# Optimization experiments

Measured on AMD Instinct MI355X. Metric: run time of the kernel, lower is better.

## Reference

```python
import jax, jax.numpy as jnp
import numpy as np

D_MODEL = 256; N_HEADS = 8; N_LEVELS = 4; N_POINTS = 4; D_FFN = 1024
BS = 8; NQ = 100; NKPT = 17
LEVEL_SHAPES = [(160, 160), (80, 80), (40, 40), (20, 20)]  # (H, W) per level
LEN_V = sum(h * w for h, w in LEVEL_SHAPES)  # 34000


def layer_norm(x, g, b, eps=1e-5):
    m = x.mean(-1, keepdims=True)
    v = ((x - m) ** 2).mean(-1, keepdims=True)
    return (x - m) * jax.lax.rsqrt(v + eps) * g + b


def mha(q, k, v, Wqkv, bqkv, Wo, bo):
    # torch nn.MultiheadAttention, batch_first, eval mode (no dropout)
    d = q.shape[-1]; dh = d // N_HEADS
    def proj(x, W, b):
        return (x @ W.T + b).reshape(*x.shape[:-1], N_HEADS, dh)
    qp = proj(q, Wqkv[:d], bqkv[:d])
    kp = proj(k, Wqkv[d:2 * d], bqkv[d:2 * d])
    vp = proj(v, Wqkv[2 * d:], bqkv[2 * d:])
    att = jnp.einsum('bqhd,bkhd->bhqk', qp, kp) / jnp.sqrt(jnp.asarray(dh, q.dtype))
    att = jax.nn.softmax(att, -1)
    out = jnp.einsum('bhqk,bkhd->bqhd', att, vp).reshape(q.shape)
    return out @ Wo.T + bo


def bilinear_sample(val, loc, h, w):
    # val: (B, H, h*w, Dh); loc: (B, Lq, H, P, 2) normalized to [0,1]
    # matches F.grid_sample(align_corners=False, padding_mode='zeros') on grid 2*loc-1
    B, Lq, H, P, _ = loc.shape
    px = loc[..., 0] * w - 0.5
    py = loc[..., 1] * h - 0.5
    x0f = jnp.floor(px); y0f = jnp.floor(py)
    lx = px - x0f; ly = py - y0f
    x0 = x0f.astype(jnp.int32); y0 = y0f.astype(jnp.int32)
    out = jnp.zeros((B, H, Lq, P, val.shape[-1]), val.dtype)
    for dx, dy, wt in ((0, 0, (1 - lx) * (1 - ly)), (1, 0, lx * (1 - ly)),
                       (0, 1, (1 - lx) * ly), (1, 1, lx * ly)):
        xi = x0 + dx; yi = y0 + dy
        valid = ((xi >= 0) & (xi < w) & (yi >= 0) & (yi < h)).astype(val.dtype)
        idx = jnp.clip(yi, 0, h - 1) * w + jnp.clip(xi, 0, w - 1)  # (B,Lq,H,P)
        idx = idx.transpose(0, 2, 1, 3).reshape(B, H, Lq * P)
        g = jnp.take_along_axis(val, idx[..., None], axis=2).reshape(B, H, Lq, P, -1)
        out = out + g * (wt * valid).transpose(0, 2, 1, 3)[..., None]
    return out  # (B, H, Lq, P, Dh)


def ms_deform_attn(query, ref_points, memory, off_W, off_b, aw_W, aw_b,
                   val_W, val_b, outp_W, outp_b):
    B, Lq, _ = query.shape
    dh = D_MODEL // N_HEADS
    value = (memory @ val_W.T + val_b).reshape(B, LEN_V, N_HEADS, dh)
    off = (query @ off_W.T + off_b).reshape(B, Lq, N_HEADS, N_LEVELS, N_POINTS, 2)
    aw = (query @ aw_W.T + aw_b).reshape(B, Lq, N_HEADS, N_LEVELS * N_POINTS)
    aw = jax.nn.softmax(aw, -1).reshape(B, Lq, N_HEADS, N_LEVELS, N_POINTS)
    normalizer = jnp.array([[w, h] for h, w in LEVEL_SHAPES], dtype=query.dtype)  # (L,2) as (W,H)
    loc = ref_points[:, :, None, :, None, :] + off / normalizer[None, None, None, :, None, :]
    out = jnp.zeros((B, Lq, N_HEADS, dh), query.dtype)
    start = 0
    for l, (h, w) in enumerate(LEVEL_SHAPES):
        vl = value[:, start:start + h * w].transpose(0, 2, 1, 3)  # (B,H,hw,Dh)
        s = bilinear_sample(vl, loc[:, :, :, l], h, w)            # (B,H,Lq,P,Dh)
        out = out + jnp.einsum('bhqpd,bqhp->bqhd', s, aw[:, :, :, l])
        start += h * w
    return out.reshape(B, Lq, D_MODEL) @ outp_W.T + outp_b


def setup_inputs() -> dict:
    key = jax.random.key(0)
    ks = iter(jax.random.split(key, 40))
    d = D_MODEL
    def w(shape, s=0.02):
        return jax.random.normal(next(ks), shape, jnp.float32) * s
    inp = {
        'tgt_pose': jax.random.normal(next(ks), (BS, NQ, NKPT, d), jnp.float32),
        'tgt_pose_query_pos': jax.random.normal(next(ks), (BS, NQ, NKPT, d), jnp.float32),
        'tgt_pose_reference_points': jax.random.uniform(next(ks), (BS, NQ * NKPT, N_LEVELS, 2), jnp.float32),
        'memory': jax.random.normal(next(ks), (BS, LEN_V, d), jnp.float32),
        'win_Wqkv': w((3 * d, d)), 'win_bqkv': jnp.zeros((3 * d,), jnp.float32),
        'win_Wo': w((d, d)), 'win_bo': jnp.zeros((d,), jnp.float32),
        'win_ng': jnp.ones((d,), jnp.float32), 'win_nb': jnp.zeros((d,), jnp.float32),
        'acr_Wqkv': w((3 * d, d)), 'acr_bqkv': jnp.zeros((3 * d,), jnp.float32),
        'acr_Wo': w((d, d)), 'acr_bo': jnp.zeros((d,), jnp.float32),
        'acr_ng': jnp.ones((d,), jnp.float32), 'acr_nb': jnp.zeros((d,), jnp.float32),
        'off_W': w((N_HEADS * N_LEVELS * N_POINTS * 2, d)),
        'off_b': jax.random.uniform(next(ks), (N_HEADS * N_LEVELS * N_POINTS * 2,), jnp.float32, -1.0, 1.0),
        'aw_W': w((N_HEADS * N_LEVELS * N_POINTS, d)), 'aw_b': jnp.zeros((N_HEADS * N_LEVELS * N_POINTS,), jnp.float32),
        'val_W': w((d, d)), 'val_b': jnp.zeros((d,), jnp.float32),
        'outp_W': w((d, d)), 'outp_b': jnp.zeros((d,), jnp.float32),
        'gate_W': w((2 * d, 2 * d)), 'gate_b': jnp.zeros((2 * d,), jnp.float32),
        'gate_ng': jnp.ones((d,), jnp.float32), 'gate_nb': jnp.zeros((d,), jnp.float32),
        'ffn_W1': w((D_FFN, d)), 'ffn_b1': jnp.zeros((D_FFN,), jnp.float32),
        'ffn_W2': w((d, D_FFN)), 'ffn_b2': jnp.zeros((d,), jnp.float32),
        'n2_g': jnp.ones((d,), jnp.float32), 'n2_b': jnp.zeros((d,), jnp.float32),
        'memory_spatial_shapes': jnp.array(LEVEL_SHAPES, jnp.int32),
    }
    return inp


def reference(tgt_pose, tgt_pose_query_pos, tgt_pose_reference_points, memory,
              win_Wqkv, win_bqkv, win_Wo, win_bo, win_ng, win_nb,
              acr_Wqkv, acr_bqkv, acr_Wo, acr_bo, acr_ng, acr_nb,
              off_W, off_b, aw_W, aw_b, val_W, val_b, outp_W, outp_b,
              gate_W, gate_b, gate_ng, gate_nb,
              ffn_W1, ffn_b1, ffn_W2, ffn_b2, n2_g, n2_b,
              memory_spatial_shapes):
    bs, nq, K, d = tgt_pose.shape
    # with_pos_embed mutates tgt_pose in place in the torch code -> residual includes pos
    tgt = tgt_pose + tgt_pose_query_pos
    # within-attention over keypoints of each query
    x = tgt.reshape(bs * nq, K, d)
    t2 = mha(x, x, x, win_Wqkv, win_bqkv, win_Wo, win_bo).reshape(bs, nq, K, d)
    tgt = layer_norm(tgt + t2, win_ng, win_nb)
    # across-attention over queries for each keypoint
    xk = tgt.transpose(0, 2, 1, 3).reshape(bs * K, nq, d)
    t2 = mha(xk, xk, xk, acr_Wqkv, acr_bqkv, acr_Wo, acr_bo)
    tgt = layer_norm(xk + t2, acr_ng, acr_nb).reshape(bs, K, nq, d).transpose(0, 2, 1, 3)
    # second in-place pos add before deformable cross-attn (also feeds gateway)
    tgt_q = tgt + tgt_pose_query_pos
    t2 = ms_deform_attn(tgt_q.reshape(bs, nq * K, d), tgt_pose_reference_points, memory,
                        off_W, off_b, aw_W, aw_b, val_W, val_b, outp_W, outp_b)
    t2 = t2.reshape(bs, nq, K, d)
    # Gate
    g = jax.nn.sigmoid(jnp.concatenate([tgt_q, t2], -1) @ gate_W.T + gate_b)
    g1, g2 = jnp.split(g, 2, -1)
    tgt = layer_norm(g1 * tgt_q + g2 * t2, gate_ng, gate_nb)
    # FFN
    h = jax.nn.relu(tgt @ ffn_W1.T + ffn_b1)
    tgt = tgt + h @ ffn_W2.T + ffn_b2
    tgt = layer_norm(jnp.clip(tgt, -65504.0, 65504.0), n2_g, n2_b)
    return tgt
```

## Files before the change

### kernel.cpp

```cpp
#include <hip/hip_runtime.h>
#include <hip/hip_bf16.h>

#define NH 8
#define BS_ 8
#define NQ_ 100
#define NK_ 17
#define LQ 1700
#define T_TOK 13600
#define LEN_VV 34000

typedef __attribute__((ext_vector_type(8))) short short8v;
typedef __attribute__((ext_vector_type(8))) __bf16 bf16x8;
typedef __attribute__((ext_vector_type(4))) float f32x4;

__device__ __forceinline__ float wave_sum(float v){
#pragma unroll
  for (int m = 32; m; m >>= 1) v += __shfl_xor(v, m, 64);
  return v;
}
__device__ __forceinline__ short f2bf(float f){
  __hip_bfloat16 h = __float2bfloat16(f);
  return *reinterpret_cast<short*>(&h);
}
__device__ __forceinline__ float bf2f(short s){
  return __uint_as_float(((uint)(unsigned short)s) << 16);
}

template<int EPI, int ADDA, int SWZ>
__global__ __launch_bounds__(256) void mgemm_k(const float* __restrict__ A,
                                               const float* __restrict__ A2,
                                               const float* __restrict__ W,
                                               const float* __restrict__ bias,
                                               __hip_bfloat16* __restrict__ Cb,
                                               int M, int N, int K, int nbx){
  __shared__ short sh[128 * 136];
  short* As = sh;
  short* Ws = sh + 128 * 64;
  int j;
  if (SWZ){
    int total = gridDim.x;
    int q = total >> 3, r = total & 7;
    int x = blockIdx.x & 7, k = blockIdx.x >> 3;
    j = (x < r) ? x * (q + 1) + k : r * (q + 1) + (x - r) * q + k;
  } else {
    j = blockIdx.x;
  }
  const int tid = threadIdx.x;
  const int bm = (j / nbx) * 128, bn = (j % nbx) * 128;
  const int wave = tid >> 6, lane = tid & 63;
  const int wm = (wave >> 1) * 64, wn = (wave & 1) * 64;
  const int s = tid & 7;
  const int row0 = tid >> 3;
  f32x4 acc[4][4] = {};
  const int lrow = lane & 15, lk = lane >> 4;

  float4 ra[8], rw[8];
#pragma unroll
  for (int i = 0; i < 4; i++){
    int row = row0 + i * 32;
    int gr = bm + row;
    float4 z = make_float4(0.f, 0.f, 0.f, 0.f);
    if (gr < M){
      const float* p = A + (size_t)gr * K + s * 8;
      float4 x0 = ((const float4*)p)[0], x1 = ((const float4*)p)[1];
      if (ADDA){
        const float* q2 = A2 + (size_t)gr * K + s * 8;
        float4 y0 = ((const float4*)q2)[0], y1 = ((const float4*)q2)[1];
        x0.x+=y0.x; x0.y+=y0.y; x0.z+=y0.z; x0.w+=y0.w;
        x1.x+=y1.x; x1.y+=y1.y; x1.z+=y1.z; x1.w+=y1.w;
      }
      ra[2 * i] = x0; ra[2 * i + 1] = x1;
    } else { ra[2 * i] = z; ra[2 * i + 1] = z; }
    const float* q = W + (size_t)(bn + row) * K + s * 8;
    rw[2 * i] = ((const float4*)q)[0]; rw[2 * i + 1] = ((const float4*)q)[1];
  }

  for (int k0 = 0; k0 < K; k0 += 64){
#pragma unroll
    for (int i = 0; i < 4; i++){
      int row = row0 + i * 32;
      int sw = ((s ^ (row & 7)) << 3) + row * 64;
      float4 a0 = ra[2 * i], a1 = ra[2 * i + 1];
      short8v v;
      v[0]=f2bf(a0.x); v[1]=f2bf(a0.y); v[2]=f2bf(a0.z); v[3]=f2bf(a0.w);
      v[4]=f2bf(a1.x); v[5]=f2bf(a1.y); v[6]=f2bf(a1.z); v[7]=f2bf(a1.w);
      *(short8v*)&As[sw] = v;
      a0 = rw[2 * i]; a1 = rw[2 * i + 1];
      short8v u;
      u[0]=f2bf(a0.x); u[1]=f2bf(a0.y); u[2]=f2bf(a0.z); u[3]=f2bf(a0.w);
      u[4]=f2bf(a1.x); u[5]=f2bf(a1.y); u[6]=f2bf(a1.z); u[7]=f2bf(a1.w);
      *(short8v*)&Ws[sw] = u;
    }
    __syncthreads();
    if (k0 + 64 < K){
#pragma unroll
      for (int i = 0; i < 4; i++){
        int row = row0 + i * 32;
        int gr = bm + row;
        float4 z = make_float4(0.f, 0.f, 0.f, 0.f);
        if (gr < M){
          const float* p = A + (size_t)gr * K + k0 + 64 + s * 8;
          float4 x0 = ((const float4*)p)[0], x1 = ((const float4*)p)[1];
          if (ADDA){
            const float* q2 = A2 + (size_t)gr * K + k0 + 64 + s * 8;
            float4 y0 = ((const float4*)q2)[0], y1 = ((const float4*)q2)[1];
            x0.x+=y0.x; x0.y+=y0.y; x0.z+=y0.z; x0.w+=y0.w;
            x1.x+=y1.x; x1.y+=y1.y; x1.z+=y1.z; x1.w+=y1.w;
          }
          ra[2 * i] = x0; ra[2 * i + 1] = x1;
        } else { ra[2 * i] = z; ra[2 * i + 1] = z; }
        const float* q = W + (size_t)(bn + row) * K + k0 + 64 + s * 8;
        rw[2 * i] = ((const float4*)q)[0]; rw[2 * i + 1] = ((const float4*)q)[1];
      }
    }
#pragma unroll
    for (int ks = 0; ks < 2; ks++){
      short8v af[4], bw[4];
      int slot = ks * 4 + lk;
#pragma unroll
      for (int m = 0; m < 4; m++){
        int r = wm + m * 16 + lrow;
        af[m] = *(const short8v*)&As[r * 64 + ((slot ^ (r & 7)) << 3)];
      }
#pragma unroll
      for (int n = 0; n < 4; n++){
        int r = wn + n * 16 + lrow;
        bw[n] = *(const short8v*)&Ws[r * 64 + ((slot ^ (r & 7)) << 3)];
      }
#pragma unroll
      for (int m = 0; m < 4; m++)
#pragma unroll
        for (int n = 0; n < 4; n++)
          acc[m][n] = __builtin_amdgcn_mfma_f32_16x16x32_bf16(
              __builtin_bit_cast(bf16x8, af[m]),
              __builtin_bit_cast(bf16x8, bw[n]), acc[m][n], 0, 0, 0);
    }
    __syncthreads();
  }
  const int STR = 136;
#pragma unroll
  for (int n = 0; n < 4; n++){
    int col = wn + n * 16 + lrow;
    float bsv = bias[bn + col];
#pragma unroll
    for (int m = 0; m < 4; m++){
#pragma unroll
      for (int i = 0; i < 4; i++){
        int row = wm + m * 16 + lk * 4 + i;
        float c = acc[m][n][i] + bsv;
        if (EPI == 1) c = fmaxf(c, 0.f);
        sh[row * STR + col] = f2bf(c);
      }
    }
  }
  __syncthreads();
#pragma unroll
  for (int it = 0; it < 8; it++){
    int r = it * 16 + (tid >> 4);
    int chunk = tid & 15;
    if (bm + r < M){
      uint4 v = *(const uint4*)((const char*)sh + r * 272 + chunk * 16);
      *(uint4*)((char*)Cb + ((size_t)(bm + r) * N + bn) * 2 + chunk * 16) = v;
    }
  }
}

template<int EPI, int OUTB, int INB, int DUALA>
__global__ __launch_bounds__(256) void g64_k(const void* __restrict__ Av,
                                             const void* __restrict__ A1v,
                                             const float* __restrict__ W0,
                                             const float* __restrict__ W1,
                                             int NSPLIT,
                                             const float* __restrict__ bias0,
                                             const float* __restrict__ bias1,
                                             const float* __restrict__ RES,
                                             float* __restrict__ Cf,
                                             __hip_bfloat16* __restrict__ Cb,
                                             int M, int N, int K, int sA){
  __shared__ short sh64[2 * 64 * 64];
  short* As = sh64;
  short* Ws = sh64 + 64 * 64;
  const int tid = threadIdx.x;
  const int bn = blockIdx.x * 64, bm = blockIdx.y * 64;
  const int wave = tid >> 6, lane = tid & 63;
  const int wm = (wave >> 1) * 32, wn = (wave & 1) * 32;
  const int s = tid & 7, row0 = tid >> 3;
  const int lrow = lane & 15, lk = lane >> 4;
  f32x4 acc[2][2] = {};

  for (int k0 = 0; k0 < K; k0 += 64){
#pragma unroll
    for (int i = 0; i < 2; i++){
      int row = row0 + i * 32;
      int sw = ((s ^ (row & 7)) << 3) + row * 64;
      short8v v = {};
      int gr = bm + row;
      if (gr < M){
        if (INB){
          v = *(const short8v*)((const short*)Av + (size_t)gr * sA + k0 + s * 8);
        } else {
          const float* Ap;
          if (DUALA) Ap = (k0 < 256) ? (const float*)Av + (size_t)gr * 256 + k0
                                     : (const float*)A1v + (size_t)gr * 256 + (k0 - 256);
          else Ap = (const float*)Av + (size_t)gr * sA + k0;
          float4 a0 = ((const float4*)(Ap + s * 8))[0];
          float4 a1 = ((const float4*)(Ap + s * 8))[1];
          v[0]=f2bf(a0.x); v[1]=f2bf(a0.y); v[2]=f2bf(a0.z); v[3]=f2bf(a0.w);
          v[4]=f2bf(a1.x); v[5]=f2bf(a1.y); v[6]=f2bf(a1.z); v[7]=f2bf(a1.w);
        }
      }
      *(short8v*)&As[sw] = v;
      int wr = bn + row;
      const float* Wp = (wr < NSPLIT) ? W0 + (size_t)wr * K + k0
                                      : W1 + (size_t)(wr - NSPLIT) * K + k0;
      float4 b0 = ((const float4*)(Wp + s * 8))[0];
      float4 b1 = ((const float4*)(Wp + s * 8))[1];
      short8v u;
      u[0]=f2bf(b0.x); u[1]=f2bf(b0.y); u[2]=f2bf(b0.z); u[3]=f2bf(b0.w);
      u[4]=f2bf(b1.x); u[5]=f2bf(b1.y); u[6]=f2bf(b1.z); u[7]=f2bf(b1.w);
      *(short8v*)&Ws[sw] = u;
    }
    __syncthreads();
#pragma unroll
    for (int ks = 0; ks < 2; ks++){
      int slot = ks * 4 + lk;
      short8v af[2], bw[2];
#pragma unroll
      for (int m = 0; m < 2; m++){
        int r = wm + m * 16 + lrow;
        af[m] = *(const short8v*)&As[r * 64 + ((slot ^ (r & 7)) << 3)];
      }
#pragma unroll
      for (int n = 0; n < 2; n++){
        int r = wn + n * 16 + lrow;
        bw[n] = *(const short8v*)&Ws[r * 64 + ((slot ^ (r & 7)) << 3)];
      }
#pragma unroll
      for (int m = 0; m < 2; m++)
#pragma unroll
        for (int n = 0; n < 2; n++)
          acc[m][n] = __builtin_amdgcn_mfma_f32_16x16x32_bf16(
              __builtin_bit_cast(bf16x8, af[m]),
              __builtin_bit_cast(bf16x8, bw[n]), acc[m][n], 0, 0, 0);
    }
    __syncthreads();
  }
  if (OUTB){
    const int STR = 72;
#pragma unroll
    for (int n = 0; n < 2; n++){
      int col = wn + n * 16 + lrow;
      int gc = bn + col;
      float bsv = (gc < NSPLIT) ? bias0[gc] : bias1[gc - NSPLIT];
#pragma unroll
      for (int m = 0; m < 2; m++){
#pragma unroll
        for (int i = 0; i < 4; i++){
          int row = wm + m * 16 + lk * 4 + i;
          float c = acc[m][n][i] + bsv;
          if (EPI == 1) c = fmaxf(c, 0.f);
          if (EPI == 2) c = 1.f / (1.f + expf(-c));
          sh64[row * STR + col] = f2bf(c);
        }
      }
    }
    __syncthreads();
#pragma unroll
    for (int it = 0; it < 2; it++){
      int r = it * 32 + (tid >> 3);
      int chunk = tid & 7;
      if (bm + r < M){
        uint4 v = *(const uint4*)((const char*)sh64 + r * 144 + chunk * 16);
        *(uint4*)((char*)Cb + ((size_t)(bm + r) * N + bn) * 2 + chunk * 16) = v;
      }
    }
  } else {
#pragma unroll
    for (int n = 0; n < 2; n++){
      int gc = bn + wn + n * 16 + lrow;
      float bsv = (gc < NSPLIT) ? bias0[gc] : bias1[gc - NSPLIT];
#pragma unroll
      for (int m = 0; m < 2; m++){
#pragma unroll
        for (int i = 0; i < 4; i++){
          int row = bm + wm + m * 16 + lk * 4 + i;
          if (row >= M) continue;
          float c = acc[m][n][i] + bsv;
          if (EPI == 1) c = fmaxf(c, 0.f);
          if (EPI == 2) c = 1.f / (1.f + expf(-c));
          if (EPI == 3) c += RES[(size_t)row * N + gc];
          Cf[(size_t)row * N + gc] = c;
        }
      }
    }
  }
}

template<int TP, int NSPL>
__global__ __launch_bounds__(256) void mha_mfma_k(const short* __restrict__ qkv,
                                                  __hip_bfloat16* __restrict__ out, int S){
  constexpr int MT = TP / 16;
  constexpr int KSTEPS = (TP + 31) / 32;
  constexpr int KS32 = KSTEPS * 32;
  constexpr int VSTRB = (KS32 == 128) ? 256 : 128;
  constexpr int CH = (MT + NSPL - 1) / NSPL;
  __shared__ short QK[2][TP][64];
  __shared__ short Vt[2][32][VSTRB / 2];
  __shared__ float Sc[2][16][128];
  __shared__ float rinv[2][16];

  const int tid = threadIdx.x;
  const int bid = blockIdx.x;
  const int batch = bid / (4 * NSPL);
  const int rem = bid % (4 * NSPL);
  const int hp = rem / NSPL;
  const int half = rem % NSPL;
  const int mtlo = half * CH;
  const int mthi = (mtlo + CH < MT) ? (mtlo + CH) : MT;
  const int wave = tid >> 6, lane = tid & 63;
  const int hh = wave >> 1, wsub = wave & 1;
  const int lrow = lane & 15, lk = lane >> 4;
  const float scale = 0.17677669529663687f;
  const size_t qbase = (size_t)batch * S * 768;

  for (int idx = tid; idx < 2 * TP * 4; idx += 256){
    int h2 = idx >= TP * 4;
    int rm = idx - h2 * TP * 4;
    int j = rm >> 2, s = rm & 3;
    int h = hp * 2 + h2;
    short8v qv = {}, kv = {};
    if (j < S){
      const short* p = qkv + qbase + (size_t)j * 768 + h * 32 + s * 8;
      qv = *(const short8v*)p;
      kv = *(const short8v*)(p + 256);
    }
    *(short8v*)&QK[h2][j][(s ^ (j & 7)) << 3] = qv;
    *(short8v*)&QK[h2][j][((s + 4) ^ (j & 7)) << 3] = kv;
  }
  for (int idx = tid; idx < 2 * KS32 * 4; idx += 256){
    int h2 = idx >= KS32 * 4;
    int rm = idx - h2 * KS32 * 4;
    int j = rm >> 2, e8 = rm & 3;
    int h = hp * 2 + h2;
    short8v v = {};
    if (j < S) v = *(const short8v*)(qkv + qbase + (size_t)j * 768 + h * 32 + 512 + e8 * 8);
#pragma unroll
    for (int c = 0; c < 8; c++){
      int e = e8 * 8 + c;
      char* pb = (char*)&Vt[h2][0][0] + e * VSTRB + (((j >> 3) ^ (e & 7)) << 4) + ((j & 7) << 1);
      *(short*)pb = v[c];
    }
  }
  __syncthreads();

  for (int mt = mtlo; mt < mthi; mt++){
    for (int nt = wsub; nt < MT; nt += 2){
      int ar = mt * 16 + lrow;
      short8v aq = *(const short8v*)&QK[hh][ar][(lk ^ (ar & 7)) << 3];
      int br = nt * 16 + lrow;
      short8v bk = *(const short8v*)&QK[hh][br][((lk + 4) ^ (br & 7)) << 3];
      f32x4 z = {};
      f32x4 d = __builtin_amdgcn_mfma_f32_16x16x32_bf16(
          __builtin_bit_cast(bf16x8, aq), __builtin_bit_cast(bf16x8, bk), z, 0, 0, 0);
#pragma unroll
      for (int i = 0; i < 4; i++){
        int rr = lk * 4 + i;
        int c = nt * 16 + lrow;
        Sc[hh][rr][(((c >> 2) ^ (rr & 7)) << 2) + (c & 3)] = d[i] * scale;
      }
    }
    __syncthreads();
    if (wsub == 0){
      int rr = lane >> 2, p = lane & 3;
      int grow = mt * 16 + rr;
      int Seff = (grow < S) ? S : 0;
      float mx = -1e30f;
#pragma unroll
      for (int m = 0; m < KSTEPS; m++){
        int j = p + 4 * m;
#pragma unroll
        for (int hf = 0; hf < 2; hf++){
          int ls = 2 * j + hf;
          float4 v = *(const float4*)&Sc[hh][rr][(ls ^ (rr & 7)) << 2];
          int c0 = ls * 4;
          mx = fmaxf(mx, (c0 + 0 < Seff) ? v.x : -1e30f);
          mx = fmaxf(mx, (c0 + 1 < Seff) ? v.y : -1e30f);
          mx = fmaxf(mx, (c0 + 2 < Seff) ? v.z : -1e30f);
          mx = fmaxf(mx, (c0 + 3 < Seff) ? v.w : -1e30f);
        }
      }
      mx = fmaxf(mx, __shfl_xor(mx, 1, 64));
      mx = fmaxf(mx, __shfl_xor(mx, 2, 64));
      float sum = 0.f;
#pragma unroll
      for (int m = 0; m < KSTEPS; m++){
        int j = p + 4 * m;
        float ev[8];
#pragma unroll
        for (int hf = 0; hf < 2; hf++){
          int ls = 2 * j + hf;
          float4 v = *(const float4*)&Sc[hh][rr][(ls ^ (rr & 7)) << 2];
          int c0 = ls * 4;
          ev[hf * 4 + 0] = (c0 + 0 < Seff) ? __expf(v.x - mx) : 0.f;
          ev[hf * 4 + 1] = (c0 + 1 < Seff) ? __expf(v.y - mx) : 0.f;
          ev[hf * 4 + 2] = (c0 + 2 < Seff) ? __expf(v.z - mx) : 0.f;
          ev[hf * 4 + 3] = (c0 + 3 < Seff) ? __expf(v.w - mx) : 0.f;
        }
        short8v pb;
#pragma unroll
        for (int q2 = 0; q2 < 8; q2++){ pb[q2] = f2bf(ev[q2]); sum += ev[q2]; }
        *(short8v*)((char*)&Sc[hh][rr][0] + ((j ^ (rr & 7)) << 4)) = pb;
      }
      sum += __shfl_xor(sum, 1, 64);
      sum += __shfl_xor(sum, 2, 64);
      if (p == 0) rinv[hh][rr] = (sum > 0.f) ? 1.f / sum : 0.f;
    }
    __syncthreads();
    {
      int nt2 = wsub;
      f32x4 acc = {};
#pragma unroll
      for (int ks = 0; ks < KSTEPS; ks++){
        int slot = ks * 4 + lk;
        short8v ap = *(const short8v*)((const char*)&Sc[hh][lrow][0] + ((slot ^ (lrow & 7)) << 4));
        int e = nt2 * 16 + lrow;
        short8v bv = *(const short8v*)((const char*)&Vt[hh][0][0] + e * VSTRB + ((slot ^ (e & 7)) << 4));
        acc = __builtin_amdgcn_mfma_f32_16x16x32_bf16(
            __builtin_bit_cast(bf16x8, ap), __builtin_bit_cast(bf16x8, bv), acc, 0, 0, 0);
      }
      int h = hp * 2 + hh;
#pragma unroll
      for (int i = 0; i < 4; i++){
        int row = mt * 16 + lk * 4 + i;
        if (row < S){
          float rv = rinv[hh][lk * 4 + i];
          out[((size_t)batch * S + row) * 256 + h * 32 + nt2 * 16 + lrow] =
              __float2bfloat16(acc[i] * rv);
        }
      }
    }
    __syncthreads();
  }
}

template<int MODE>
__global__ __launch_bounds__(64) void ln_k(const float* __restrict__ a,
                                           const float* __restrict__ b,
                                           const float* __restrict__ g,
                                           const float* __restrict__ be,
                                           float* __restrict__ out,
                                           const float* __restrict__ qpre,
                                           const float* __restrict__ qpost){
  int r = blockIdx.x;
  int lane = threadIdx.x;
  float4 xa = *(const float4*)(a + (size_t)r * 256 + lane * 4);
  float x[4] = { xa.x, xa.y, xa.z, xa.w };
  if (MODE != 5){
    float4 xb = *(const float4*)(b + (size_t)r * 256 + lane * 4);
    x[0] += xb.x; x[1] += xb.y; x[2] += xb.z; x[3] += xb.w;
  }
  if (MODE == 4){
    float4 xq = *(const float4*)(qpre + (size_t)r * 256 + lane * 4);
    x[0] += xq.x; x[1] += xq.y; x[2] += xq.z; x[3] += xq.w;
  }
  if (MODE == 5){
#pragma unroll
    for (int i = 0; i < 4; i++) x[i] = fminf(fmaxf(x[i], -65504.f), 65504.f);
  }
  float s = x[0] + x[1] + x[2] + x[3];
  s = wave_sum(s);
  float mean = s * (1.f / 256.f);
  float sq = 0.f;
#pragma unroll
  for (int i = 0; i < 4; i++){ float d = x[i] - mean; sq += d * d; }
  float var = wave_sum(sq) * (1.f / 256.f);
  float rstd = rsqrtf(var + 1e-5f);
  float4 gg = *(const float4*)(g + lane * 4);
  float4 bb = *(const float4*)(be + lane * 4);
  size_t orow = r;
  if (MODE == 3){
    int bi = r / LQ; int rem = r % LQ; int kk = rem / NQ_; int q = rem % NQ_;
    orow = (size_t)bi * LQ + q * NK_ + kk;
  }
  if (MODE == 4){
    int bi = r / LQ; int rem = r % LQ; int q = rem / NK_; int kk = rem % NK_;
    orow = (size_t)bi * LQ + kk * NQ_ + q;
  }
  float4 o;
  o.x = (x[0] - mean) * rstd * gg.x + bb.x;
  o.y = (x[1] - mean) * rstd * gg.y + bb.y;
  o.z = (x[2] - mean) * rstd * gg.z + bb.z;
  o.w = (x[3] - mean) * rstd * gg.w + bb.w;
  if (MODE == 3){
    float4 qv = *(const float4*)(qpost + orow * 256 + lane * 4);
    o.x += qv.x; o.y += qv.y; o.z += qv.z; o.w += qv.w;
  }
  *(float4*)(out + orow * 256 + lane * 4) = o;
}

__global__ __launch_bounds__(64) void gate_ln_k(const short* __restrict__ G,
                                                const float* __restrict__ aq,
                                                const float* __restrict__ t2,
                                                const float* __restrict__ g,
                                                const float* __restrict__ be,
                                                float* __restrict__ out){
  int r = blockIdx.x;
  int lane = threadIdx.x;
  const short* gp = G + (size_t)r * 512 + lane * 4;
  float g1v[4], g2v[4];
#pragma unroll
  for (int i = 0; i < 4; i++){ g1v[i] = bf2f(gp[i]); g2v[i] = bf2f(gp[256 + i]); }
  float4 xa = *(const float4*)(aq + (size_t)r * 256 + lane * 4);
  float4 xt = *(const float4*)(t2 + (size_t)r * 256 + lane * 4);
  float x[4] = { g1v[0] * xa.x + g2v[0] * xt.x, g1v[1] * xa.y + g2v[1] * xt.y,
                 g1v[2] * xa.z + g2v[2] * xt.z, g1v[3] * xa.w + g2v[3] * xt.w };
  float s = x[0] + x[1] + x[2] + x[3];
  s = wave_sum(s);
  float mean = s * (1.f / 256.f);
  float sq = 0.f;
#pragma unroll
  for (int i = 0; i < 4; i++){ float d = x[i] - mean; sq += d * d; }
  float var = wave_sum(sq) * (1.f / 256.f);
  float rstd = rsqrtf(var + 1e-5f);
  float4 gg = *(const float4*)(g + lane * 4);
  float4 bb = *(const float4*)(be + lane * 4);
  float4 o;
  o.x = (x[0] - mean) * rstd * gg.x + bb.x;
  o.y = (x[1] - mean) * rstd * gg.y + bb.y;
  o.z = (x[2] - mean) * rstd * gg.z + bb.z;
  o.w = (x[3] - mean) * rstd * gg.w + bb.w;
  *(float4*)(out + (size_t)r * 256 + lane * 4) = o;
}

__global__ __launch_bounds__(256) void deform_k(const __hip_bfloat16* __restrict__ val,
                                                const float* __restrict__ offaw,
                                                const float* __restrict__ ref,
                                                unsigned int* __restrict__ outb){
  __shared__ uint2 meta[32][16][4];
  const int tid = threadIdx.x;
  const int t0 = blockIdx.x * 4;
  {
    int g = tid >> 3;
    int pair = tid & 7;
    int lt = g >> 3, h = g & 7;
    int t = t0 + lt;
    int b = t / LQ;
    int p0 = pair * 2;
    int l = p0 >> 2;
    const int starts[4] = {0, 25600, 32000, 33600};
    const int HS[4] = {160, 80, 40, 20};
    int w = HS[l];
    const float* ap = offaw + (size_t)t * 384 + 256 + h * 16;
    float a0 = ap[p0];
    float a1 = ap[p0 + 1];
    float mx = fmaxf(a0, a1);
#pragma unroll
    for (int m = 1; m <= 4; m <<= 1) mx = fmaxf(mx, __shfl_xor(mx, m, 64));
    float e0 = expf(a0 - mx), e1 = expf(a1 - mx);
    float s = e0 + e1;
#pragma unroll
    for (int m = 1; m <= 4; m <<= 1) s += __shfl_xor(s, m, 64);
    float inv = 1.f / s;
    float rx = ref[((size_t)t * 4 + l) * 2 + 0];
    float ry = ref[((size_t)t * 4 + l) * 2 + 1];
    float4 ov = *(const float4*)(offaw + (size_t)t * 384 + h * 32 + l * 8 + p0 * 2);
    int vbase = (b * LEN_VV + starts[l]) * 128 + h * 16;
#pragma unroll
    for (int pp = 0; pp < 2; pp++){
      float wgt = (pp ? e1 : e0) * inv;
      float px = rx * w + (pp ? ov.z : ov.x) - 0.5f;
      float py = ry * w + (pp ? ov.w : ov.y) - 0.5f;
      float x0f = floorf(px), y0f = floorf(py);
      float lx = px - x0f, ly = py - y0f;
      int x0 = (int)x0f, y0 = (int)y0f;
#pragma unroll
    for (int c = 0; c < 4; c++){
        int dx = c & 1, dy = c >> 1;
        int xi = x0 + dx, yi = y0 + dy;
        bool ok = (xi >= 0) & (xi < w) & (yi >= 0) & (yi < w);
        float cw = ok ? wgt * (dx ? lx : 1.f - lx) * (dy ? ly : 1.f - ly) : 0.f;
        uint idx = ok ? (uint)(vbase + (yi * w + xi) * 128) : 0u;
        uint2 m2; m2.x = idx; m2.y = __float_as_uint(cw);
        meta[g][p0 + pp][c] = m2;
      }
    }
  }
  __syncthreads();
  const uint* V2 = (const uint*)val;
  int sg = tid >> 4, lane = tid & 15;
#pragma unroll
  for (int it = 0; it < 2; it++){
    int g = it * 16 + sg;
    int lt = g >> 3, h = g & 7;
    int t = t0 + lt;
    float ax = 0.f, ay = 0.f;
#pragma unroll 4
    for (int c = 0; c < 64; c++){
      uint2 mw = meta[g][c >> 2][c & 3];
      float wv = __uint_as_float(mw.y);
      uint v = V2[(size_t)mw.x + lane];
      float lo = __uint_as_float(v << 16);
      float hi = __uint_as_float(v & 0xffff0000u);
      ax += wv * lo;
      ay += wv * hi;
    }
    uint u = ((uint)(unsigned short)f2bf(ay) << 16) | (uint)(unsigned short)f2bf(ax);
    outb[((size_t)t * 256 + h * 32) / 2 + lane] = u;
  }
}

extern "C" void kernel_launch(void* const* d_in, const int* in_sizes, int n_in,
                              void* d_out, int out_size, void* d_ws, size_t ws_size,
                              hipStream_t stream){
  const float* tgt_pose = (const float*)d_in[0];
  const float* qpos     = (const float*)d_in[1];
  const float* refp     = (const float*)d_in[2];
  const float* memory   = (const float*)d_in[3];
  const float* win_Wqkv = (const float*)d_in[4];
  const float* win_bqkv = (const float*)d_in[5];
  const float* win_Wo   = (const float*)d_in[6];
  const float* win_bo   = (const float*)d_in[7];
  const float* win_ng   = (const float*)d_in[8];
  const float* win_nb   = (const float*)d_in[9];
  const float* acr_Wqkv = (const float*)d_in[10];
  const float* acr_bqkv = (const float*)d_in[11];
  const float* acr_Wo   = (const float*)d_in[12];
  const float* acr_bo   = (const float*)d_in[13];
  const float* acr_ng   = (const float*)d_in[14];
  const float* acr_nb   = (const float*)d_in[15];
  const float* off_W    = (const float*)d_in[16];
  const float* off_b    = (const float*)d_in[17];
  const float* aw_W     = (const float*)d_in[18];
  const float* aw_b     = (const float*)d_in[19];
  const float* val_W    = (const float*)d_in[20];
  const float* val_b    = (const float*)d_in[21];
  const float* outp_W   = (const float*)d_in[22];
  const float* outp_b   = (const float*)d_in[23];
  const float* gate_W   = (const float*)d_in[24];
  const float* gate_b   = (const float*)d_in[25];
  const float* gate_ng  = (const float*)d_in[26];
  const float* gate_nb  = (const float*)d_in[27];
  const float* ffn_W1   = (const float*)d_in[28];
  const float* ffn_b1   = (const float*)d_in[29];
  const float* ffn_W2   = (const float*)d_in[30];
  const float* ffn_b2   = (const float*)d_in[31];
  const float* n2_g     = (const float*)d_in[32];
  const float* n2_b     = (const float*)d_in[33];

  float* out = (float*)d_out;
  char* ws = (char*)d_ws;
  const size_t TB = (size_t)T_TOK * 256 * 4;
  float* B0 = (float*)(ws);
  float* B1 = (float*)(ws + TB);
  float* B2 = (float*)(ws + 2 * TB);
  float* B3 = (float*)(ws + 3 * TB);
  char* p = ws + 4 * TB;
  short* Qb = (short*)p;                 p += (size_t)T_TOK * 768 * 2;
  short* ABF = (short*)p;                p += (size_t)T_TOK * 256 * 2;
  float* OFFAW = (float*)p;              p += (size_t)T_TOK * 384 * 4;
  short* Gb = (short*)p;                 p += (size_t)T_TOK * 512 * 2;
  char* Vregion = p;
  __hip_bfloat16* V = (__hip_bfloat16*)Vregion;
  short* FF = (short*)Vregion;

  const int GM128 = (T_TOK + 127) / 128;
  const int GM64  = (T_TOK + 63) / 64;
  const int BIG = 1 << 30;

  mgemm_k<0,0,1><<<2 * 2125, 256, 0, stream>>>(memory, nullptr, val_W, val_b, V, BS_ * LEN_VV, 256, 256, 2);
  mgemm_k<0,1,0><<<6 * GM128, 256, 0, stream>>>(tgt_pose, qpos, win_Wqkv, win_bqkv, (__hip_bfloat16*)Qb, T_TOK, 768, 256, 6);
  mha_mfma_k<32,1><<<800 * 4, 256, 0, stream>>>(Qb, (__hip_bfloat16*)ABF, 17);
  g64_k<0,0,1,0><<<dim3(4, GM64), 256, 0, stream>>>(ABF, nullptr, win_Wo, win_Wo, BIG, win_bo, win_bo, nullptr, B2, nullptr, T_TOK, 256, 256, 256);
  ln_k<4><<<T_TOK, 64, 0, stream>>>(tgt_pose, B2, win_ng, win_nb, B1, qpos, nullptr);
  mgemm_k<0,0,0><<<6 * GM128, 256, 0, stream>>>(B1, nullptr, acr_Wqkv, acr_bqkv, (__hip_bfloat16*)Qb, T_TOK, 768, 256, 6);
  mha_mfma_k<112,2><<<136 * 8, 256, 0, stream>>>(Qb, (__hip_bfloat16*)ABF, 100);
  g64_k<0,0,1,0><<<dim3(4, GM64), 256, 0, stream>>>(ABF, nullptr, acr_Wo, acr_Wo, BIG, acr_bo, acr_bo, nullptr, B2, nullptr, T_TOK, 256, 256, 256);
  ln_k<3><<<T_TOK, 64, 0, stream>>>(B1, B2, acr_ng, acr_nb, B0, nullptr, qpos);
  g64_k<0,0,0,0><<<dim3(6, GM64), 256, 0, stream>>>(B0, nullptr, off_W, aw_W, 256, off_b, aw_b, nullptr, OFFAW, nullptr, T_TOK, 384, 256, 256);
  deform_k<<<T_TOK / 4, 256, 0, stream>>>(V, OFFAW, refp, (unsigned int*)ABF);
  g64_k<0,0,1,0><<<dim3(4, GM64), 256, 0, stream>>>(ABF, nullptr, outp_W, outp_W, BIG, outp_b, outp_b, nullptr, B3, nullptr, T_TOK, 256, 256, 256);
  g64_k<2,1,0,1><<<dim3(8, GM64), 256, 0, stream>>>(B0, B3, gate_W, gate_W, BIG, gate_b, gate_b, nullptr, nullptr, (__hip_bfloat16*)Gb, T_TOK, 512, 512, 256);
  gate_ln_k<<<T_TOK, 64, 0, stream>>>(Gb, B0, B3, gate_ng, gate_nb, B2);
  mgemm_k<1,0,0><<<8 * GM128, 256, 0, stream>>>(B2, nullptr, ffn_W1, ffn_b1, (__hip_bfloat16*)FF, T_TOK, 1024, 256, 8);
  g64_k<3,0,1,0><<<dim3(4, GM64), 256, 0, stream>>>(FF, nullptr, ffn_W2, ffn_W2, BIG, ffn_b2, ffn_b2, B2, B1, nullptr, T_TOK, 256, 1024, 1024);
  ln_k<5><<<T_TOK, 64, 0, stream>>>(B1, nullptr, n2_g, n2_b, out, nullptr, nullptr);
}
```

Before: 472.6 us.

## Fuse output-projection GEMMs with residual LayerNorm and widen deform gather loads

Adds a 512-thread GEMM kernel whose block computes a full 256-wide output row tile, then applies bias, residual adds, optional clamp, LayerNorm and the transposed row remap in the epilogue. It replaces three GEMM plus LayerNorm kernel pairs, removing the fp32 intermediate round-trip and three launches. It also changes the deform sampling gather so each lane loads 4 bf16 values (uint2) with 8 lanes per head instead of 2 values with 16 lanes. Risks: the fused kernel launches only one block per 64 rows (about 213 blocks), so there is less parallelism, it converts fp32 weights to bf16 inside every block, and it computes variance with the single-pass E[x²]−mean² formula.

```diff
diff --git a/kernel.cpp b/kernel.cpp
--- a/kernel.cpp
+++ b/kernel.cpp
@@ -296,6 +296,148 @@
   }
 }
 
+template<int SITE>
+__global__ __launch_bounds__(512) void gln_k(const short* __restrict__ Abf,
+                                             const float* __restrict__ W,
+                                             const float* __restrict__ bias,
+                                             const float* __restrict__ r0,
+                                             const float* __restrict__ r1,
+                                             const float* __restrict__ g,
+                                             const float* __restrict__ be,
+                                             float* __restrict__ out,
+                                             int M, int K){
+  __shared__ short As[64 * 64];
+  __shared__ short Ws[256 * 64];
+  __shared__ float part[64][4][2];
+  __shared__ float stats[64][2];
+  const int tid = threadIdx.x;
+  const int bm = blockIdx.x * 64;
+  const int wave = tid >> 6, lane = tid & 63;
+  const int wm = (wave >> 2) * 32, wn = (wave & 3) * 64;
+  const int s = tid & 7, row0 = tid >> 3;
+  const int lrow = lane & 15, lk = lane >> 4;
+  f32x4 acc[2][4] = {};
+
+  short8v pa = {};
+  { int gr = bm + row0; if (gr < M) pa = *(const short8v*)(Abf + (size_t)gr * K + s * 8); }
+  float4 pw[8];
+#pragma unroll
+  for (int i = 0; i < 4; i++){
+    const float* wp = W + (size_t)(row0 + i * 64) * K + s * 8;
+    pw[2 * i] = ((const float4*)wp)[0]; pw[2 * i + 1] = ((const float4*)wp)[1];
+  }
+
+  for (int k0 = 0; k0 < K; k0 += 64){
+    *(short8v*)&As[row0 * 64 + ((s ^ (row0 & 7)) << 3)] = pa;
+#pragma unroll
+    for (int i = 0; i < 4; i++){
+      int row = row0 + i * 64;
+      float4 b0 = pw[2 * i], b1 = pw[2 * i + 1];
+      short8v u;
+      u[0]=f2bf(b0.x); u[1]=f2bf(b0.y); u[2]=f2bf(b0.z); u[3]=f2bf(b0.w);
+      u[4]=f2bf(b1.x); u[5]=f2bf(b1.y); u[6]=f2bf(b1.z); u[7]=f2bf(b1.w);
+      *(short8v*)&Ws[row * 64 + ((s ^ (row & 7)) << 3)] = u;
+    }
+    __syncthreads();
+    if (k0 + 64 < K){
+      int gr = bm + row0;
+      pa = (short8v){};
+      if (gr < M) pa = *(const short8v*)(Abf + (size_t)gr * K + k0 + 64 + s * 8);
+#pragma unroll
+      for (int i = 0; i < 4; i++){
+        const float* wp = W + (size_t)(row0 + i * 64) * K + k0 + 64 + s * 8;
+        pw[2 * i] = ((const float4*)wp)[0]; pw[2 * i + 1] = ((const float4*)wp)[1];
+      }
+    }
+#pragma unroll
+    for (int ks = 0; ks < 2; ks++){
+      int slot = ks * 4 + lk;
+      short8v af[2], bw[4];
+#pragma unroll
+      for (int m = 0; m < 2; m++){
+        int r = wm + m * 16 + lrow;
+        af[m] = *(const short8v*)&As[r * 64 + ((slot ^ (r & 7)) << 3)];
+      }
+#pragma unroll
+      for (int n = 0; n < 4; n++){
+        int r = wn + n * 16 + lrow;
+        bw[n] = *(const short8v*)&Ws[r * 64 + ((slot ^ (r & 7)) << 3)];
+      }
+#pragma unroll
+      for (int m = 0; m < 2; m++)
+#pragma unroll
+        for (int n = 0; n < 4; n++)
+          acc[m][n] = __builtin_amdgcn_mfma_f32_16x16x32_bf16(
+              __builtin_bit_cast(bf16x8, af[m]),
+              __builtin_bit_cast(bf16x8, bw[n]), acc[m][n], 0, 0, 0);
+    }
+    __syncthreads();
+  }
+
+#pragma unroll
+  for (int m = 0; m < 2; m++){
+#pragma unroll
+    for (int i = 0; i < 4; i++){
+      int row = wm + m * 16 + lk * 4 + i;
+      int grow = bm + row;
+      float s1 = 0.f, s2 = 0.f;
+      if (grow < M){
+#pragma unroll
+        for (int n = 0; n < 4; n++){
+          int col = wn + n * 16 + lrow;
+          float x = acc[m][n][i] + bias[col] + r0[(size_t)grow * 256 + col];
+          if (SITE == 0) x += r1[(size_t)grow * 256 + col];
+          if (SITE == 2) x = fminf(fmaxf(x, -65504.f), 65504.f);
+          acc[m][n][i] = x;
+          s1 += x; s2 += x * x;
+        }
+      }
+#pragma unroll
+      for (int msk = 1; msk <= 8; msk <<= 1){
+        s1 += __shfl_xor(s1, msk, 64);
+        s2 += __shfl_xor(s2, msk, 64);
+      }
+      if (lrow == 0){ part[row][wave & 3][0] = s1; part[row][wave & 3][1] = s2; }
+    }
+  }
+  __syncthreads();
+  if (tid < 64){
+    float s1 = part[tid][0][0] + part[tid][1][0] + part[tid][2][0] + part[tid][3][0];
+    float s2 = part[tid][0][1] + part[tid][1][1] + part[tid][2][1] + part[tid][3][1];
+    float mean = s1 * (1.f / 256.f);
+    float var = s2 * (1.f / 256.f) - mean * mean;
+    stats[tid][0] = mean;
+    stats[tid][1] = rsqrtf(fmaxf(var, 0.f) + 1e-5f);
+  }
+  __syncthreads();
+#pragma unroll
+  for (int m = 0; m < 2; m++){
+#pragma unroll
+    for (int i = 0; i < 4; i++){
+      int row = wm + m * 16 + lk * 4 + i;
+      int grow = bm + row;
+      if (grow >= M) continue;
+      float mean = stats[row][0], rstd = stats[row][1];
+      size_t orow = grow;
+      if (SITE == 0){
+        int bi = grow / LQ; int rem = grow % LQ; int q = rem / NK_; int kk = rem % NK_;
+        orow = (size_t)bi * LQ + kk * NQ_ + q;
+      }
+      if (SITE == 1){
+        int bi = grow / LQ; int rem = grow % LQ; int kk = rem / NQ_; int q = rem % NQ_;
+        orow = (size_t)bi * LQ + q * NK_ + kk;
+      }
+#pragma unroll
+      for (int n = 0; n < 4; n++){
+        int col = wn + n * 16 + lrow;
+        float o = (acc[m][n][i] - mean) * rstd * g[col] + be[col];
+        if (SITE == 1) o += r1[orow * 256 + col];
+        out[orow * 256 + col] = o;
+      }
+    }
+  }
+}
+
 template<int TP, int NSPL>
 __global__ __launch_bounds__(256) void mha_mfma_k(const short* __restrict__ qkv,
                                                   __hip_bfloat16* __restrict__ out, int S){
@@ -441,61 +583,6 @@
     }
     __syncthreads();
   }
-}
-
-template<int MODE>
-__global__ __launch_bounds__(64) void ln_k(const float* __restrict__ a,
-                                           const float* __restrict__ b,
-                                           const float* __restrict__ g,
-                                           const float* __restrict__ be,
-                                           float* __restrict__ out,
-                                           const float* __restrict__ qpre,
-                                           const float* __restrict__ qpost){
-  int r = blockIdx.x;
-  int lane = threadIdx.x;
-  float4 xa = *(const float4*)(a + (size_t)r * 256 + lane * 4);
-  float x[4] = { xa.x, xa.y, xa.z, xa.w };
-  if (MODE != 5){
-    float4 xb = *(const float4*)(b + (size_t)r * 256 + lane * 4);
-    x[0] += xb.x; x[1] += xb.y; x[2] += xb.z; x[3] += xb.w;
-  }
-  if (MODE == 4){
-    float4 xq = *(const float4*)(qpre + (size_t)r * 256 + lane * 4);
-    x[0] += xq.x; x[1] += xq.y; x[2] += xq.z; x[3] += xq.w;
-  }
-  if (MODE == 5){
-#pragma unroll
-    for (int i = 0; i < 4; i++) x[i] = fminf(fmaxf(x[i], -65504.f), 65504.f);
-  }
-  float s = x[0] + x[1] + x[2] + x[3];
-  s = wave_sum(s);
-  float mean = s * (1.f / 256.f);
-  float sq = 0.f;
-#pragma unroll
-  for (int i = 0; i < 4; i++){ float d = x[i] - mean; sq += d * d; }
-  float var = wave_sum(sq) * (1.f / 256.f);
-  float rstd = rsqrtf(var + 1e-5f);
-  float4 gg = *(const float4*)(g + lane * 4);
-  float4 bb = *(const float4*)(be + lane * 4);
-  size_t orow = r;
-  if (MODE == 3){
-    int bi = r / LQ; int rem = r % LQ; int kk = rem / NQ_; int q = rem % NQ_;
-    orow = (size_t)bi * LQ + q * NK_ + kk;
-  }
-  if (MODE == 4){
-    int bi = r / LQ; int rem = r % LQ; int q = rem / NK_; int kk = rem % NK_;
-    orow = (size_t)bi * LQ + kk * NQ_ + q;
-  }
-  float4 o;
-  o.x = (x[0] - mean) * rstd * gg.x + bb.x;
-  o.y = (x[1] - mean) * rstd * gg.y + bb.y;
-  o.z = (x[2] - mean) * rstd * gg.z + bb.z;
-  o.w = (x[3] - mean) * rstd * gg.w + bb.w;
-  if (MODE == 3){
-    float4 qv = *(const float4*)(qpost + orow * 256 + lane * 4);
-    o.x += qv.x; o.y += qv.y; o.z += qv.z; o.w += qv.w;
-  }
-  *(float4*)(out + orow * 256 + lane * 4) = o;
 }
 
 __global__ __launch_bounds__(64) void gate_ln_k(const short* __restrict__ G,
@@ -574,7 +661,7 @@
       float lx = px - x0f, ly = py - y0f;
       int x0 = (int)x0f, y0 = (int)y0f;
 #pragma unroll
-    for (int c = 0; c < 4; c++){
+      for (int c = 0; c < 4; c++){
         int dx = c & 1, dy = c >> 1;
         int xi = x0 + dx, yi = y0 + dy;
         bool ok = (xi >= 0) & (xi < w) & (yi >= 0) & (yi < w);
@@ -586,27 +673,25 @@
     }
   }
   __syncthreads();
-  const uint* V2 = (const uint*)val;
-  int sg = tid >> 4, lane = tid & 15;
-#pragma unroll
-  for (int it = 0; it < 2; it++){
-    int g = it * 16 + sg;
-    int lt = g >> 3, h = g & 7;
-    int t = t0 + lt;
-    float ax = 0.f, ay = 0.f;
+  const uint2* V2 = (const uint2*)val;
+  int sg = tid >> 3, lane8 = tid & 7;
+  int lt = sg >> 3, h = sg & 7;
+  int t = t0 + lt;
+  float a0 = 0.f, a1 = 0.f, a2 = 0.f, a3 = 0.f;
 #pragma unroll 4
-    for (int c = 0; c < 64; c++){
-      uint2 mw = meta[g][c >> 2][c & 3];
-      float wv = __uint_as_float(mw.y);
-      uint v = V2[(size_t)mw.x + lane];
-      float lo = __uint_as_float(v << 16);
-      float hi = __uint_as_float(v & 0xffff0000u);
-      ax += wv * lo;
-      ay += wv * hi;
-    }
-    uint u = ((uint)(unsigned short)f2bf(ay) << 16) | (uint)(unsigned short)f2bf(ax);
-    outb[((size_t)t * 256 + h * 32) / 2 + lane] = u;
-  }
+  for (int c = 0; c < 64; c++){
+    uint2 mw = meta[sg][c >> 2][c & 3];
+    float wv = __uint_as_float(mw.y);
+    uint2 v = V2[(size_t)(mw.x >> 1) + lane8];
+    a0 += wv * __uint_as_float(v.x << 16);
+    a1 += wv * __uint_as_float(v.x & 0xffff0000u);
+    a2 += wv * __uint_as_float(v.y << 16);
+    a3 += wv * __uint_as_float(v.y & 0xffff0000u);
+  }
+  uint2 u;
+  u.x = ((uint)(unsigned short)f2bf(a1) << 16) | (uint)(unsigned short)f2bf(a0);
+  u.y = ((uint)(unsigned short)f2bf(a3) << 16) | (uint)(unsigned short)f2bf(a2);
+  ((uint2*)outb)[((size_t)t * 256 + h * 32) / 4 + lane8] = u;
 }
 
 extern "C" void kernel_launch(void* const* d_in, const int* in_sizes, int n_in,
@@ -670,18 +755,15 @@
   mgemm_k<0,0,1><<<2 * 2125, 256, 0, stream>>>(memory, nullptr, val_W, val_b, V, BS_ * LEN_VV, 256, 256, 2);
   mgemm_k<0,1,0><<<6 * GM128, 256, 0, stream>>>(tgt_pose, qpos, win_Wqkv, win_bqkv, (__hip_bfloat16*)Qb, T_TOK, 768, 256, 6);
   mha_mfma_k<32,1><<<800 * 4, 256, 0, stream>>>(Qb, (__hip_bfloat16*)ABF, 17);
-  g64_k<0,0,1,0><<<dim3(4, GM64), 256, 0, stream>>>(ABF, nullptr, win_Wo, win_Wo, BIG, win_bo, win_bo, nullptr, B2, nullptr, T_TOK, 256, 256, 256);
-  ln_k<4><<<T_TOK, 64, 0, stream>>>(tgt_pose, B2, win_ng, win_nb, B1, qpos, nullptr);
+  gln_k<0><<<GM64, 512, 0, stream>>>(ABF, win_Wo, win_bo, tgt_pose, qpos, win_ng, win_nb, B1, T_TOK, 256);
   mgemm_k<0,0,0><<<6 * GM128, 256, 0, stream>>>(B1, nullptr, acr_Wqkv, acr_bqkv, (__hip_bfloat16*)Qb, T_TOK, 768, 256, 6);
   mha_mfma_k<112,2><<<136 * 8, 256, 0, stream>>>(Qb, (__hip_bfloat16*)ABF, 100);
-  g64_k<0,0,1,0><<<dim3(4, GM64), 256, 0, stream>>>(ABF, nullptr, acr_Wo, acr_Wo, BIG, acr_bo, acr_bo, nullptr, B2, nullptr, T_TOK, 256, 256, 256);
-  ln_k<3><<<T_TOK, 64, 0, stream>>>(B1, B2, acr_ng, acr_nb, B0, nullptr, qpos);
+  gln_k<1><<<GM64, 512, 0, stream>>>(ABF, acr_Wo, acr_bo, B1, qpos, acr_ng, acr_nb, B0, T_TOK, 256);
   g64_k<0,0,0,0><<<dim3(6, GM64), 256, 0, stream>>>(B0, nullptr, off_W, aw_W, 256, off_b, aw_b, nullptr, OFFAW, nullptr, T_TOK, 384, 256, 256);
   deform_k<<<T_TOK / 4, 256, 0, stream>>>(V, OFFAW, refp, (unsigned int*)ABF);
   g64_k<0,0,1,0><<<dim3(4, GM64), 256, 0, stream>>>(ABF, nullptr, outp_W, outp_W, BIG, outp_b, outp_b, nullptr, B3, nullptr, T_TOK, 256, 256, 256);
   g64_k<2,1,0,1><<<dim3(8, GM64), 256, 0, stream>>>(B0, B3, gate_W, gate_W, BIG, gate_b, gate_b, nullptr, nullptr, (__hip_bfloat16*)Gb, T_TOK, 512, 512, 256);
   gate_ln_k<<<T_TOK, 64, 0, stream>>>(Gb, B0, B3, gate_ng, gate_nb, B2);
   mgemm_k<1,0,0><<<8 * GM128, 256, 0, stream>>>(B2, nullptr, ffn_W1, ffn_b1, (__hip_bfloat16*)FF, T_TOK, 1024, 256, 8);
-  g64_k<3,0,1,0><<<dim3(4, GM64), 256, 0, stream>>>(FF, nullptr, ffn_W2, ffn_W2, BIG, ffn_b2, ffn_b2, B2, B1, nullptr, T_TOK, 256, 1024, 1024);
-  ln_k<5><<<T_TOK, 64, 0, stream>>>(B1, nullptr, n2_g, n2_b, out, nullptr, nullptr);
-}
+  gln_k<2><<<GM64, 512, 0, stream>>>(FF, ffn_W2, ffn_b2, B2, nullptr, n2_g, n2_b, out, T_TOK, 1024);
+}
```

Result: no change. 467.3 us (-1.1%).
